# Kernel optimization log

Measured on AMD Instinct MI355X. Metric: run time of the kernel, lower is better.

The kernel has to match this reference:

```python
import jax, jax.numpy as jnp
import numpy as np

NODE_NUMS = 128
IN_SIZE = 256
OUT_SIZE = 256
BATCH = 4096


def setup_inputs() -> dict:
    key = jax.random.key(0)
    k1, k2, k3, k4, k5 = jax.random.split(key, 5)
    # Xavier-uniform bounds
    limit_w = float(np.sqrt(6.0 / (IN_SIZE + OUT_SIZE)))
    limit_b = float(np.sqrt(6.0 / (NODE_NUMS + OUT_SIZE)))
    x = jax.random.normal(k1, (BATCH, IN_SIZE), dtype=jnp.float32)
    var_vector = jax.random.normal(k2, (BATCH, 16), dtype=jnp.float32)  # unused in forward
    W_1 = jax.random.uniform(k3, (NODE_NUMS, IN_SIZE, OUT_SIZE), dtype=jnp.float32,
                             minval=-limit_w, maxval=limit_w)
    b_1 = jax.random.uniform(k4, (NODE_NUMS, OUT_SIZE), dtype=jnp.float32,
                             minval=-limit_b, maxval=limit_b)
    node_ind = jax.random.randint(k5, (2, BATCH), 0, NODE_NUMS, dtype=jnp.int32)
    return {"x": x, "var_vector": var_vector, "W_1": W_1, "b_1": b_1, "node_ind": node_ind}


def reference(x, var_vector, W_1, b_1, node_ind):
    # idx selects a per-sample expert (node) weight matrix and bias.
    idx = node_ind[1]                       # [B]
    W = W_1[idx]                            # [B, in, out] gathered weights
    b = b_1[idx]                            # [B, out]
    # bmm(x[:,None,:], W).squeeze() + b  ==  einsum over the input dim
    return jnp.einsum('bi,bio->bo', x, W) + b
```

## Files before the change

kernel.cpp:

```cpp
#include <hip/hip_runtime.h>

#define BATCH 4096
#define INS   256
#define OUTS  256
#define NODES 128
#define NT    64
#define MCH   32
#define PITCH 264

typedef short short8 __attribute__((ext_vector_type(8)));
typedef short short4v __attribute__((ext_vector_type(4)));
typedef float f32x4  __attribute__((ext_vector_type(4)));

struct SMem {
    unsigned short wt[NT * PITCH];
    unsigned short list[BATCH];
    int cnt;
};

__device__ __forceinline__ unsigned short f2bf(float f) {
    unsigned int u = __builtin_bit_cast(unsigned int, f);
    u += 0x7fffu + ((u >> 16) & 1u);
    return (unsigned short)(u >> 16);
}

__device__ __forceinline__ short8 pack8(float4 a, float4 b) {
    short8 r;
    r[0] = (short)f2bf(a.x); r[1] = (short)f2bf(a.y);
    r[2] = (short)f2bf(a.z); r[3] = (short)f2bf(a.w);
    r[4] = (short)f2bf(b.x); r[5] = (short)f2bf(b.y);
    r[6] = (short)f2bf(b.z); r[7] = (short)f2bf(b.w);
    return r;
}

__global__ __launch_bounds__(256, 3) void moe_fwd(
    const float* __restrict__ x, const float* __restrict__ W1,
    const float* __restrict__ b1, const int* __restrict__ nid,
    float* __restrict__ out)
{
    __shared__ SMem sm;
    const int t   = threadIdx.x;
    const int bid = blockIdx.x;
    const int sub = bid >> 3;
    const int e   = (bid & 7) * 16 + (sub >> 2);
    const int c0  = (sub & 3) * NT;

    const int w  = t >> 6;
    const int l  = t & 63;
    const int g  = l >> 4;
    const int ln = l & 15;
    const int cc = c0 + w * 16 + ln;

    if (t == 0) sm.cnt = 0;
    __syncthreads();

    const float* __restrict__ wgp = W1 + (size_t)e * (INS * OUTS) + c0;
    {
        const int c4 = (t & 15) * 4;
        const int kq = (t >> 4) * 4;
        #pragma unroll
        for (int pass = 0; pass < 4; ++pass) {
            const int kb = pass * 64 + kq;
            f32x4 v0 = __builtin_nontemporal_load(
                reinterpret_cast<const f32x4*>(&wgp[(size_t)(kb + 0) * OUTS + c4]));
            f32x4 v1 = __builtin_nontemporal_load(
                reinterpret_cast<const f32x4*>(&wgp[(size_t)(kb + 1) * OUTS + c4]));
            f32x4 v2 = __builtin_nontemporal_load(
                reinterpret_cast<const f32x4*>(&wgp[(size_t)(kb + 2) * OUTS + c4]));
            f32x4 v3 = __builtin_nontemporal_load(
                reinterpret_cast<const f32x4*>(&wgp[(size_t)(kb + 3) * OUTS + c4]));
            #pragma unroll
            for (int ci = 0; ci < 4; ++ci) {
                short4v s;
                s[0] = (short)f2bf(v0[ci]);
                s[1] = (short)f2bf(v1[ci]);
                s[2] = (short)f2bf(v2[ci]);
                s[3] = (short)f2bf(v3[ci]);
                *reinterpret_cast<short4v*>(&sm.wt[(c4 + ci) * PITCH + kb]) = s;
            }
        }
    }
    const float bval = b1[e * OUTS + cc];

    const int* __restrict__ idxp = nid + BATCH;
    #pragma unroll
    for (int it = 0; it < BATCH / 256; ++it) {
        int b = it * 256 + t;
        if (idxp[b] == e) {
            int p = atomicAdd(&sm.cnt, 1);
            sm.list[p] = (unsigned short)b;
        }
    }
    asm volatile("s_waitcnt lgkmcnt(0)" ::: "memory");
    __builtin_amdgcn_s_barrier();
    asm volatile("" ::: "memory");

    const int cnt = sm.cnt;
    if (cnt == 0) return;

    for (int m0 = 0; m0 < cnt; m0 += MCH) {
        int r0 = m0 + ln;
        int r1 = m0 + 16 + ln;
        int s0 = sm.list[r0 < cnt ? r0 : cnt - 1];
        int s1 = sm.list[r1 < cnt ? r1 : cnt - 1];
        const float* __restrict__ xp0 = x + (size_t)s0 * INS + g * 8;
        const float* __restrict__ xp1 = x + (size_t)s1 * INS + g * 8;

        f32x4 acc0 = {0.f, 0.f, 0.f, 0.f};
        f32x4 acc1 = {0.f, 0.f, 0.f, 0.f};
        #pragma unroll
        for (int ks = 0; ks < 8; ++ks) {
            float4 u0 = *reinterpret_cast<const float4*>(xp0 + ks * 32);
            float4 u1 = *reinterpret_cast<const float4*>(xp0 + ks * 32 + 4);
            float4 v0 = *reinterpret_cast<const float4*>(xp1 + ks * 32);
            float4 v1 = *reinterpret_cast<const float4*>(xp1 + ks * 32 + 4);
            short8 a0 = pack8(u0, u1);
            short8 a1 = pack8(v0, v1);
            short8 bb = *reinterpret_cast<const short8*>(
                &sm.wt[(w * 16 + ln) * PITCH + ks * 32 + g * 8]);
            acc0 = __builtin_amdgcn_mfma_f32_16x16x32_bf16(a0, bb, acc0, 0, 0, 0);
            acc1 = __builtin_amdgcn_mfma_f32_16x16x32_bf16(a1, bb, acc1, 0, 0, 0);
        }

        #pragma unroll
        for (int q = 0; q < 4; ++q) {
            int rr0 = m0 + g * 4 + q;
            if (rr0 < cnt)
                __builtin_nontemporal_store(acc0[q] + bval,
                    &out[(size_t)sm.list[rr0] * OUTS + cc]);
            int rr1 = m0 + 16 + g * 4 + q;
            if (rr1 < cnt)
                __builtin_nontemporal_store(acc1[q] + bval,
                    &out[(size_t)sm.list[rr1] * OUTS + cc]);
        }
    }
}

extern "C" void kernel_launch(void* const* d_in, const int* in_sizes, int n_in,
                              void* d_out, int out_size, void* d_ws, size_t ws_size,
                              hipStream_t stream) {
    const float* x   = (const float*)d_in[0];
    const float* W1  = (const float*)d_in[2];
    const float* b1  = (const float*)d_in[3];
    const int*   nid = (const int*)d_in[4];
    float* out = (float*)d_out;

    hipLaunchKernelGGL(moe_fwd, dim3(NODES * (OUTS / NT)), dim3(256), 0, stream,
                       x, W1, b1, nid, out);
}
```

Before: 22.23 us.

## Prefetch token rows into registers and overlap weight loads with routing scan

Moves the expert-weight global loads until after the token-routing scan, so blocks with no assigned tokens skip loading weights. Weights are held in registers while the first chunk of x rows is prefetched, then converted to bf16 into shared memory. The main loop is software-pipelined with a double-buffered register prefetch of the next 16-row chunk of x. To fit the larger register footprint, the chunk size drops from 32 to 16 rows and occupancy is lowered from 3 to 2 blocks per CU.

```diff
diff --git a/kernel.cpp b/kernel.cpp
--- a/kernel.cpp
+++ b/kernel.cpp
@@ -5,7 +5,7 @@
 #define OUTS  256
 #define NODES 128
 #define NT    64
-#define MCH   32
+#define MCH   16
 #define PITCH 264
 
 typedef short short8 __attribute__((ext_vector_type(8)));
@@ -24,16 +24,36 @@
     return (unsigned short)(u >> 16);
 }
 
-__device__ __forceinline__ short8 pack8(float4 a, float4 b) {
+__device__ __forceinline__ short8 pack8(f32x4 a, f32x4 b) {
     short8 r;
-    r[0] = (short)f2bf(a.x); r[1] = (short)f2bf(a.y);
-    r[2] = (short)f2bf(a.z); r[3] = (short)f2bf(a.w);
-    r[4] = (short)f2bf(b.x); r[5] = (short)f2bf(b.y);
-    r[6] = (short)f2bf(b.z); r[7] = (short)f2bf(b.w);
+    r[0] = (short)f2bf(a[0]); r[1] = (short)f2bf(a[1]);
+    r[2] = (short)f2bf(a[2]); r[3] = (short)f2bf(a[3]);
+    r[4] = (short)f2bf(b[0]); r[5] = (short)f2bf(b[1]);
+    r[6] = (short)f2bf(b[2]); r[7] = (short)f2bf(b[3]);
     return r;
 }
 
-__global__ __launch_bounds__(256, 3) void moe_fwd(
+__device__ __forceinline__ void pf_x(const float* __restrict__ x,
+                                     const unsigned short* lst, int m0, int hi,
+                                     int ln, int g, f32x4 xr[8][2]) {
+    int r = m0 + ln;
+    if (r < hi) {
+        const float* __restrict__ xp = x + (size_t)lst[r] * INS + g * 8;
+        #pragma unroll
+        for (int ks = 0; ks < 8; ++ks) {
+            xr[ks][0] = *reinterpret_cast<const f32x4*>(xp + ks * 32);
+            xr[ks][1] = *reinterpret_cast<const f32x4*>(xp + ks * 32 + 4);
+        }
+    } else {
+        #pragma unroll
+        for (int ks = 0; ks < 8; ++ks) {
+            xr[ks][0] = (f32x4){0.f, 0.f, 0.f, 0.f};
+            xr[ks][1] = (f32x4){0.f, 0.f, 0.f, 0.f};
+        }
+    }
+}
+
+__global__ __launch_bounds__(256, 2) void moe_fwd(
     const float* __restrict__ x, const float* __restrict__ W1,
     const float* __restrict__ b1, const int* __restrict__ nid,
     float* __restrict__ out)
@@ -54,34 +74,6 @@
     if (t == 0) sm.cnt = 0;
     __syncthreads();
 
-    const float* __restrict__ wgp = W1 + (size_t)e * (INS * OUTS) + c0;
-    {
-        const int c4 = (t & 15) * 4;
-        const int kq = (t >> 4) * 4;
-        #pragma unroll
-        for (int pass = 0; pass < 4; ++pass) {
-            const int kb = pass * 64 + kq;
-            f32x4 v0 = __builtin_nontemporal_load(
-                reinterpret_cast<const f32x4*>(&wgp[(size_t)(kb + 0) * OUTS + c4]));
-            f32x4 v1 = __builtin_nontemporal_load(
-                reinterpret_cast<const f32x4*>(&wgp[(size_t)(kb + 1) * OUTS + c4]));
-            f32x4 v2 = __builtin_nontemporal_load(
-                reinterpret_cast<const f32x4*>(&wgp[(size_t)(kb + 2) * OUTS + c4]));
-            f32x4 v3 = __builtin_nontemporal_load(
-                reinterpret_cast<const f32x4*>(&wgp[(size_t)(kb + 3) * OUTS + c4]));
-            #pragma unroll
-            for (int ci = 0; ci < 4; ++ci) {
-                short4v s;
-                s[0] = (short)f2bf(v0[ci]);
-                s[1] = (short)f2bf(v1[ci]);
-                s[2] = (short)f2bf(v2[ci]);
-                s[3] = (short)f2bf(v3[ci]);
-                *reinterpret_cast<short4v*>(&sm.wt[(c4 + ci) * PITCH + kb]) = s;
-            }
-        }
-    }
-    const float bval = b1[e * OUTS + cc];
-
     const int* __restrict__ idxp = nid + BATCH;
     #pragma unroll
     for (int it = 0; it < BATCH / 256; ++it) {
@@ -98,40 +90,67 @@
     const int cnt = sm.cnt;
     if (cnt == 0) return;
 
+    const float* __restrict__ wgp = W1 + (size_t)e * (INS * OUTS) + c0;
+    const int c4 = (t & 15) * 4;
+    const int kq = (t >> 4) * 4;
+    f32x4 wr[16];
+    #pragma unroll
+    for (int pass = 0; pass < 4; ++pass) {
+        const int kb = pass * 64 + kq;
+        #pragma unroll
+        for (int j = 0; j < 4; ++j)
+            wr[pass * 4 + j] = __builtin_nontemporal_load(
+                reinterpret_cast<const f32x4*>(&wgp[(size_t)(kb + j) * OUTS + c4]));
+    }
+    const float bval = b1[e * OUTS + cc];
+
+    f32x4 xA[8][2], xB[8][2];
+    pf_x(x, sm.list, 0, cnt, ln, g, xA);
+
+    #pragma unroll
+    for (int pass = 0; pass < 4; ++pass) {
+        const int kb = pass * 64 + kq;
+        #pragma unroll
+        for (int ci = 0; ci < 4; ++ci) {
+            short4v s;
+            s[0] = (short)f2bf(wr[pass * 4 + 0][ci]);
+            s[1] = (short)f2bf(wr[pass * 4 + 1][ci]);
+            s[2] = (short)f2bf(wr[pass * 4 + 2][ci]);
+            s[3] = (short)f2bf(wr[pass * 4 + 3][ci]);
+            *reinterpret_cast<short4v*>(&sm.wt[(c4 + ci) * PITCH + kb]) = s;
+        }
+    }
+    asm volatile("s_waitcnt lgkmcnt(0)" ::: "memory");
+    __builtin_amdgcn_s_barrier();
+    asm volatile("" ::: "memory");
+
     for (int m0 = 0; m0 < cnt; m0 += MCH) {
-        int r0 = m0 + ln;
-        int r1 = m0 + 16 + ln;
-        int s0 = sm.list[r0 < cnt ? r0 : cnt - 1];
-        int s1 = sm.list[r1 < cnt ? r1 : cnt - 1];
-        const float* __restrict__ xp0 = x + (size_t)s0 * INS + g * 8;
-        const float* __restrict__ xp1 = x + (size_t)s1 * INS + g * 8;
+        const bool more = (m0 + MCH) < cnt;
+        if (more) pf_x(x, sm.list, m0 + MCH, cnt, ln, g, xB);
 
-        f32x4 acc0 = {0.f, 0.f, 0.f, 0.f};
-        f32x4 acc1 = {0.f, 0.f, 0.f, 0.f};
+        f32x4 acc = {0.f, 0.f, 0.f, 0.f};
         #pragma unroll
         for (int ks = 0; ks < 8; ++ks) {
-            float4 u0 = *reinterpret_cast<const float4*>(xp0 + ks * 32);
-            float4 u1 = *reinterpret_cast<const float4*>(xp0 + ks * 32 + 4);
-            float4 v0 = *reinterpret_cast<const float4*>(xp1 + ks * 32);
-            float4 v1 = *reinterpret_cast<const float4*>(xp1 + ks * 32 + 4);
-            short8 a0 = pack8(u0, u1);
-            short8 a1 = pack8(v0, v1);
+            short8 a0 = pack8(xA[ks][0], xA[ks][1]);
             short8 bb = *reinterpret_cast<const short8*>(
                 &sm.wt[(w * 16 + ln) * PITCH + ks * 32 + g * 8]);
-            acc0 = __builtin_amdgcn_mfma_f32_16x16x32_bf16(a0, bb, acc0, 0, 0, 0);
-            acc1 = __builtin_amdgcn_mfma_f32_16x16x32_bf16(a1, bb, acc1, 0, 0, 0);
+            acc = __builtin_amdgcn_mfma_f32_16x16x32_bf16(a0, bb, acc, 0, 0, 0);
         }
 
         #pragma unroll
         for (int q = 0; q < 4; ++q) {
-            int rr0 = m0 + g * 4 + q;
-            if (rr0 < cnt)
-                __builtin_nontemporal_store(acc0[q] + bval,
-                    &out[(size_t)sm.list[rr0] * OUTS + cc]);
-            int rr1 = m0 + 16 + g * 4 + q;
-            if (rr1 < cnt)
-                __builtin_nontemporal_store(acc1[q] + bval,
-                    &out[(size_t)sm.list[rr1] * OUTS + cc]);
+            int rr = m0 + g * 4 + q;
+            if (rr < cnt)
+                __builtin_nontemporal_store(acc[q] + bval,
+                    &out[(size_t)sm.list[rr] * OUTS + cc]);
+        }
+
+        if (more) {
+            #pragma unroll
+            for (int ks = 0; ks < 8; ++ks) {
+                xA[ks][0] = xB[ks][0];
+                xA[ks][1] = xB[ks][1];
+            }
         }
     }
 }
```

After: 21.62 us, median of 2. 1.03x faster.
